# Optimization experiments

Measured on AMD Instinct MI355X. Metric: run time of the kernel, lower is better.

Reference implementation:

```python
import jax, jax.numpy as jnp
import numpy as np

B, S, E, H = 4, 2048, 2048, 16
D = E // H  # head_dim = 128


def setup_inputs() -> dict:
    key = jax.random.key(0)
    kx, kq, kk, kv = jax.random.split(key, 4)
    std = 1.0 / np.sqrt(E)
    return {
        "x": jax.random.normal(kx, (B, S, E), dtype=jnp.float32),
        "Wq": jax.random.normal(kq, (E, E), dtype=jnp.float32) * std,
        "Wk": jax.random.normal(kk, (E, E), dtype=jnp.float32) * std,
        "Wv": jax.random.normal(kv, (E, E), dtype=jnp.float32) * std,
    }


def reference(x, Wq, Wk, Wv):
    b, s, _ = x.shape
    # nn.Linear(bias=False): y = x @ W.T
    q = (x @ Wq.T).reshape(b, s, H, D).transpose(0, 2, 1, 3)  # [b,h,s,d]
    k = (x @ Wk.T).reshape(b, s, H, D).transpose(0, 2, 1, 3)
    v = (x @ Wv.T).reshape(b, s, H, D).transpose(0, 2, 1, 3)
    scale = jnp.sqrt(jnp.asarray(D, dtype=jnp.float32))
    scores = jnp.einsum("bhqd,bhkd->bhqk", q, k) / scale  # [b,h,s,s]
    causal = jnp.tril(jnp.ones((s, s), dtype=bool))
    scores = jnp.where(causal, scores, -jnp.inf)
    weights = jax.nn.softmax(scores, axis=-1)
    attn = jnp.einsum("bhqk,bhkd->bhqd", weights, v)  # [b,h,s,d]
    return attn
```

## Files before the change

### kernel.cpp

```cpp
#include <hip/hip_runtime.h>
#include <hip/hip_bf16.h>
#include <stdint.h>

#define Bdim 4
#define Sdim 2048
#define Edim 2048
#define Hdim 16
#define Ddim 128

typedef unsigned short u16;
typedef unsigned int u32;
typedef __attribute__((ext_vector_type(8))) short bf16x8;
typedef __attribute__((ext_vector_type(4))) float f32x4;
typedef __attribute__((ext_vector_type(16))) float f32x16;
typedef __attribute__((ext_vector_type(4))) unsigned short u16x4;
typedef __attribute__((ext_vector_type(2))) unsigned int u32x2;

__device__ inline u16 f2bf(float f) {
  union { float f; uint32_t u; } v; v.f = f;
  uint32_t u = v.u;
  return (u16)((u + 0x7FFFu + ((u >> 16) & 1u)) >> 16);
}

__device__ inline u32 pkbf(float lo, float hi) {
  float2 t; t.x = lo; t.y = hi;
  union { __hip_bfloat162 h2; u32 u; } cv;
  cv.h2 = __float22bfloat162_rn(t);
  return cv.u;
}

__device__ inline f32x4 mfma16(bf16x8 a, bf16x8 b, f32x4 c) {
  return __builtin_amdgcn_mfma_f32_16x16x32_bf16(a, b, c, 0, 0, 0);
}
__device__ inline f32x16 mfma32(bf16x8 a, bf16x8 b, f32x16 c) {
  return __builtin_amdgcn_mfma_f32_32x32x16_bf16(a, b, c, 0, 0, 0);
}

__device__ inline void load_lds16(const void* g, const void* l) {
  __builtin_amdgcn_global_load_lds(
      (__attribute__((address_space(1))) void*)(uintptr_t)g,
      (__attribute__((address_space(3))) void*)(uint32_t)(uintptr_t)l,
      16, 0, 0);
}

__global__ void cvt_kernel(const float* __restrict__ src, u16* __restrict__ dst,
                           int n4, float scale) {
  int i = blockIdx.x * blockDim.x + threadIdx.x;
  if (i < n4) {
    float4 f = ((const float4*)src)[i];
    u16x4 o = { f2bf(f.x * scale), f2bf(f.y * scale),
                f2bf(f.z * scale), f2bf(f.w * scale) };
    ((u16x4*)dst)[i] = o;
  }
}

__global__ void cvt_w_kernel(const float* __restrict__ Wq,
                             const float* __restrict__ Wk,
                             const float* __restrict__ Wv,
                             u16* __restrict__ dst, float qscale) {
  int i = blockIdx.x * blockDim.x + threadIdx.x;
  int seg = i >> 20;
  int off = i & 1048575;
  const float* src = seg == 0 ? Wq : (seg == 1 ? Wk : Wv);
  float sc = seg == 0 ? qscale : 1.0f;
  float4 f = ((const float4*)src)[off];
  u16x4 o = { f2bf(f.x * sc), f2bf(f.y * sc), f2bf(f.z * sc), f2bf(f.w * sc) };
  ((u16x4*)dst)[i] = o;
}

template <bool TRANSV>
__global__ __launch_bounds__(512, 2)
void gemm_nt(const u16* __restrict__ A, const u16* __restrict__ Bw,
             u16* __restrict__ C, int M, int N, int K) {
  __shared__ char lds[131072];

  const int tid = threadIdx.x;
  const int lane = tid & 63;
  const int w = tid >> 6;
  const int wm = w >> 2, wn = w & 3;
  const int bm = blockIdx.x, bn = blockIdx.y;
  const int NT = K >> 5;

  const int srow_off = lane >> 2;
  const int schunk = lane & 3;

  const int l15 = lane & 15;
  const int l4 = lane >> 4;
  const int rA = wm * 128 + l15;
  const int rB = wn * 64 + l15;
  const int gA = (rA + (rA >> 2)) & 3;
  const int gB = (rB + (rB >> 2)) & 3;
  const int aoff = rA * 64 + ((l4 ^ gA) << 4);
  const int boff = rB * 64 + ((l4 ^ gB) << 4);

  const u16* Agp = A + (size_t)(bm * 256) * K;
  const u16* Bgp = Bw + (size_t)(bn * 256) * K;

  f32x4 acc[8][4];
#pragma unroll
  for (int m = 0; m < 8; ++m)
#pragma unroll
    for (int n = 0; n < 4; ++n)
      acc[m][n] = (f32x4){0.f, 0.f, 0.f, 0.f};

#define GSTAGE_A(tt)                                                           \
  {                                                                            \
    char* ab_ = lds + ((tt) & 3) * 16384;                                      \
    _Pragma("unroll")                                                          \
    for (int i_ = 0; i_ < 2; ++i_) {                                           \
      const int rbase_ = w * 32 + i_ * 16;                                     \
      const int row_ = rbase_ + srow_off;                                      \
      const int src_ = schunk ^ ((row_ + (row_ >> 2)) & 3);                    \
      load_lds16(Agp + (size_t)row_ * K + (tt) * 32 + src_ * 8,                \
                 ab_ + rbase_ * 64);                                           \
    }                                                                          \
  }
#define GSTAGE_B(tt)                                                           \
  {                                                                            \
    char* bb_ = lds + 65536 + ((tt) & 3) * 16384;                              \
    _Pragma("unroll")                                                          \
    for (int i_ = 0; i_ < 2; ++i_) {                                           \
      const int rbase_ = w * 32 + i_ * 16;                                     \
      const int row_ = rbase_ + srow_off;                                      \
      const int src_ = schunk ^ ((row_ + (row_ >> 2)) & 3);                    \
      load_lds16(Bgp + (size_t)row_ * K + (tt) * 32 + src_ * 8,                \
                 bb_ + rbase_ * 64);                                           \
    }                                                                          \
  }

  GSTAGE_A(0); GSTAGE_B(0);
  GSTAGE_A(1); GSTAGE_B(1);
  asm volatile("s_waitcnt vmcnt(4)" ::: "memory");
  __builtin_amdgcn_s_barrier();

  for (int t = 0; t < NT; ++t) {
    const char* ab = lds + (t & 3) * 16384 + aoff;
    const char* bb = lds + 65536 + (t & 3) * 16384 + boff;
    const bool pf = (t + 2 < NT);

    bf16x8 bfr[4], afr[4];
#pragma unroll
    for (int n = 0; n < 4; ++n) bfr[n] = *(const bf16x8*)(bb + n * 1024);
#pragma unroll
    for (int m = 0; m < 4; ++m) afr[m] = *(const bf16x8*)(ab + m * 1024);
    if (pf) GSTAGE_A(t + 2);
    __builtin_amdgcn_s_barrier();
    __builtin_amdgcn_s_setprio(1);
#pragma unroll
    for (int m = 0; m < 4; ++m)
#pragma unroll
      for (int n = 0; n < 4; ++n) acc[m][n] = mfma16(afr[m], bfr[n], acc[m][n]);
    __builtin_amdgcn_s_setprio(0);
    __builtin_amdgcn_s_barrier();

#pragma unroll
    for (int m = 0; m < 4; ++m) afr[m] = *(const bf16x8*)(ab + (m + 4) * 1024);
    if (pf) GSTAGE_B(t + 2);
    __builtin_amdgcn_s_barrier();
    __builtin_amdgcn_s_setprio(1);
#pragma unroll
    for (int m = 0; m < 4; ++m)
#pragma unroll
      for (int n = 0; n < 4; ++n)
        acc[m + 4][n] = mfma16(afr[m], bfr[n], acc[m + 4][n]);
    __builtin_amdgcn_s_setprio(0);
    if (pf) {
      asm volatile("s_waitcnt vmcnt(4)" ::: "memory");
    } else {
      asm volatile("s_waitcnt vmcnt(0)" ::: "memory");
    }
    __builtin_amdgcn_s_barrier();
  }
#undef GSTAGE_A
#undef GSTAGE_B

  const int r0 = bm * 256 + wm * 128 + (l4 << 2);
  const int c0 = bn * 256 + wn * 64 + l15;
  if (!TRANSV) {
#pragma unroll
    for (int m = 0; m < 8; ++m)
#pragma unroll
      for (int n = 0; n < 4; ++n) {
        int r = r0 + m * 16;
        int c = c0 + n * 16;
#pragma unroll
        for (int j = 0; j < 4; ++j)
          C[(size_t)(r + j) * N + c] = f2bf(acc[m][n][j]);
      }
  } else {
#pragma unroll
    for (int m = 0; m < 8; ++m)
#pragma unroll
      for (int n = 0; n < 4; ++n) {
        int ng = c0 + n * 16;
        int h = ng >> 7, d = ng & 127;
        int mg = r0 + m * 16;
        int b = mg >> 11, s = mg & 2047;
        u16x4 pk = { f2bf(acc[m][n][0]), f2bf(acc[m][n][1]),
                     f2bf(acc[m][n][2]), f2bf(acc[m][n][3]) };
        *(u16x4*)(C + ((size_t)((b * Hdim + h) * Ddim + d)) * Sdim + s) = pk;
      }
  }
}

__global__ __launch_bounds__(256)
void attn_kernel(const u16* __restrict__ Q, const u16* __restrict__ K,
                 const u16* __restrict__ Vt, float* __restrict__ O) {
  __shared__ u16 Ks[2][64 * 128];
  __shared__ u16 Vs[2][128 * 64];

  const int tid = threadIdx.x;
  const int lane = tid & 63;
  const int w = tid >> 6;
  const int l31 = lane & 31;
  const int hi = lane >> 5;

  const int bid = blockIdx.x;
  const int bh = bid & 63;
  const int qg = 15 - (bid >> 6);
  const int q0 = qg * 128;
  const int qw0 = q0 + w * 32;
  const int b = bh >> 4, h = bh & 15;

  const u16* Qb = Q + (size_t)b * Sdim * Edim + h * Ddim;
  const u16* Kb = K + (size_t)b * Sdim * Edim + h * Ddim;
  const u16* Vb = Vt + (size_t)bh * Ddim * Sdim;

  bf16x8 qf[8];
  {
    const u16* qrow = Qb + (size_t)(qw0 + l31) * Edim + hi * 8;
#pragma unroll
    for (int c = 0; c < 8; ++c) qf[c] = *(const bf16x8*)(qrow + c * 16);
  }

  f32x16 oacc[4];
#pragma unroll
  for (int d = 0; d < 4; ++d)
#pragma unroll
    for (int i = 0; i < 16; ++i) oacc[d][i] = 0.f;
  f32x16 lacc;
#pragma unroll
  for (int i = 0; i < 16; ++i) lacc[i] = 0.f;

  const short oneb = (short)0x3F80;
  const bf16x8 ones = {oneb, oneb, oneb, oneb, oneb, oneb, oneb, oneb};

  float m2 = -1e30f;
  const int qrel = qw0 + l31;

  const int nt = 2 * qg + 2;
  const int ntw = (qw0 + 31) / 64 + 1;

  const int krow_off = (lane >> 4);
  const int kchunk = lane & 15;
  const int vrow_off = (lane >> 3);
  const int vchunk = lane & 7;

#define STAGE(bufi, tt)                                                        \
  {                                                                            \
    const int kv0s = (tt) * 64;                                                \
    _Pragma("unroll")                                                          \
    for (int i = 0; i < 4; ++i) {                                              \
      const int rbase = w * 16 + i * 4;                                        \
      const int row = rbase + krow_off;                                        \
      const int cs = kchunk ^ (row & 15);                                      \
      load_lds16(Kb + (size_t)(kv0s + row) * Edim + cs * 8,                    \
                 &Ks[bufi][rbase * 128]);                                      \
    }                                                                          \
    _Pragma("unroll")                                                          \
    for (int i = 0; i < 4; ++i) {                                              \
      const int rbase = w * 32 + i * 8;                                        \
      const int row = rbase + vrow_off;                                        \
      const int cs = vchunk ^ (row & 7);                                       \
      load_lds16(Vb + (size_t)row * Sdim + kv0s + cs * 8,                      \
                 &Vs[bufi][rbase * 64]);                                       \
    }                                                                          \
  }

  STAGE(0, 0);
  __syncthreads();

  for (int t = 0; t < nt; ++t) {
    const int cur = t & 1;
    if (t + 1 < nt) STAGE(cur ^ 1, t + 1);

    if (t < ntw) {
      const int kv0 = t * 64;

      f32x16 sc0, sc1;
#pragma unroll
      for (int i = 0; i < 16; ++i) { sc0[i] = 0.f; sc1[i] = 0.f; }
      __builtin_amdgcn_s_setprio(1);
#pragma unroll
      for (int c = 0; c < 8; ++c) {
        const int ch = c * 2 + hi;
        const int r0r = l31;
        const int r1r = 32 + l31;
        bf16x8 kf0 = *(const bf16x8*)&Ks[cur][r0r * 128 + (ch ^ (r0r & 15)) * 8];
        bf16x8 kf1 = *(const bf16x8*)&Ks[cur][r1r * 128 + (ch ^ (r1r & 15)) * 8];
        sc0 = mfma32(kf0, qf[c], sc0);
        sc1 = mfma32(kf1, qf[c], sc1);
      }
      __builtin_amdgcn_s_setprio(0);

      float psc[32];
      float ma = -1e30f, mb = -1e30f, mc = -1e30f, md = -1e30f;
      if (kv0 + 64 > qw0) {
#pragma unroll
        for (int r = 0; r < 16; ++r) {
          const int cr = (r & 3) + 8 * (r >> 2) + 4 * hi;
          float v0 = (kv0 + cr <= qrel) ? sc0[r] : -1e30f;
          float v1 = (kv0 + 32 + cr <= qrel) ? sc1[r] : -1e30f;
          psc[r] = v0; psc[16 + r] = v1;
          if ((r & 3) == 0) { ma = fmaxf(fmaxf(ma, v0), v1); }
          else if ((r & 3) == 1) { mb = fmaxf(fmaxf(mb, v0), v1); }
          else if ((r & 3) == 2) { mc = fmaxf(fmaxf(mc, v0), v1); }
          else { md = fmaxf(fmaxf(md, v0), v1); }
        }
      } else {
#pragma unroll
        for (int r = 0; r < 16; ++r) {
          float v0 = sc0[r];
          float v1 = sc1[r];
          psc[r] = v0; psc[16 + r] = v1;
          if ((r & 3) == 0) { ma = fmaxf(fmaxf(ma, v0), v1); }
          else if ((r & 3) == 1) { mb = fmaxf(fmaxf(mb, v0), v1); }
          else if ((r & 3) == 2) { mc = fmaxf(fmaxf(mc, v0), v1); }
          else { md = fmaxf(fmaxf(md, v0), v1); }
        }
      }
      float mt = fmaxf(fmaxf(ma, mb), fmaxf(mc, md));
      u32x2 mx = __builtin_amdgcn_permlane32_swap(
          __float_as_uint(mt), __float_as_uint(mt), false, false);
      float mo = fmaxf(__uint_as_float(mx.x), __uint_as_float(mx.y));

      if (__any(mo - m2 > 8.0f)) {
        float mnew = fmaxf(m2, mo);
        float corr = __builtin_amdgcn_exp2f(m2 - mnew);
        m2 = mnew;
        lacc[0] *= corr;
#pragma unroll
        for (int d = 0; d < 4; ++d)
#pragma unroll
          for (int i = 0; i < 16; ++i) oacc[d][i] *= corr;
      }

#pragma unroll
      for (int r = 0; r < 32; ++r)
        psc[r] = __builtin_amdgcn_exp2f(psc[r] - m2);

      u32 pk[16];
#pragma unroll
      for (int i = 0; i < 16; ++i) pk[i] = pkbf(psc[2 * i], psc[2 * i + 1]);
      bf16x8 pa[4];
#pragma unroll
      for (int t2 = 0; t2 < 2; ++t2)
#pragma unroll
        for (int q2 = 0; q2 < 2; ++q2) {
          const int base = t2 * 8 + q2 * 4;
          u32x2 r0 = __builtin_amdgcn_permlane32_swap(pk[base + 0], pk[base + 2],
                                                      false, false);
          u32x2 r1 = __builtin_amdgcn_permlane32_swap(pk[base + 1], pk[base + 3],
                                                      false, false);
          union { u32 wv[4]; bf16x8 v; } cv;
          cv.wv[0] = r0.x; cv.wv[1] = r1.x; cv.wv[2] = r0.y; cv.wv[3] = r1.y;
          pa[t2 * 2 + q2] = cv.v;
        }

      __builtin_amdgcn_s_setprio(1);
#pragma unroll
      for (int dblk = 0; dblk < 4; ++dblk) {
        const int row = dblk * 32 + l31;
#pragma unroll
        for (int ks = 0; ks < 4; ++ks) {
          const int ch = ks * 2 + hi;
          bf16x8 vf = *(const bf16x8*)&Vs[cur][row * 64 + (ch ^ (row & 7)) * 8];
          oacc[dblk] = mfma32(vf, pa[ks], oacc[dblk]);
        }
      }
#pragma unroll
      for (int ks = 0; ks < 4; ++ks) lacc = mfma32(ones, pa[ks], lacc);
      __builtin_amdgcn_s_setprio(0);
    }

    __syncthreads();
  }
#undef STAGE

  float inv = 1.0f / lacc[0];
  float* Ob = O + ((size_t)bh * Sdim + qw0 + l31) * Ddim + hi * 4;
#pragma unroll
  for (int dblk = 0; dblk < 4; ++dblk)
#pragma unroll
    for (int g = 0; g < 4; ++g) {
      f32x4 o4 = { oacc[dblk][4 * g] * inv, oacc[dblk][4 * g + 1] * inv,
                   oacc[dblk][4 * g + 2] * inv, oacc[dblk][4 * g + 3] * inv };
      *(f32x4*)(Ob + dblk * 32 + g * 8) = o4;
    }
}

extern "C" void kernel_launch(void* const* d_in, const int* in_sizes, int n_in,
                              void* d_out, int out_size, void* d_ws, size_t ws_size,
                              hipStream_t stream) {
  const float* x  = (const float*)d_in[0];
  const float* Wq = (const float*)d_in[1];
  const float* Wk = (const float*)d_in[2];
  const float* Wv = (const float*)d_in[3];
  float* out = (float*)d_out;
  char* ws = (char*)d_ws;

  u16* xb  = (u16*)(ws);
  u16* wqb = (u16*)(ws + 33554432ull);
  u16* wkb = (u16*)(ws + 41943040ull);
  u16* wvb = (u16*)(ws + 50331648ull);
  u16* Qb  = (u16*)(ws + 58720256ull);
  u16* Kb  = (u16*)(ws + 92274688ull);
  u16* Vt  = (u16*)(ws + 125829120ull);

  const int nX = Bdim * Sdim * Edim;
  const int nW = Edim * Edim;
  const float K1SC = 0.08838834764831845f * 1.4426950408889634f;
  cvt_kernel<<<(nX / 4 + 255) / 256, 256, 0, stream>>>(x, xb, nX / 4, 1.0f);
  cvt_w_kernel<<<(3 * nW / 4 + 255) / 256, 256, 0, stream>>>(Wq, Wk, Wv, wqb, K1SC);

  dim3 g(Bdim * Sdim / 256, Edim / 256);
  gemm_nt<false><<<g, 512, 0, stream>>>(xb, wqb, Qb, Bdim * Sdim, Edim, Edim);
  gemm_nt<false><<<g, 512, 0, stream>>>(xb, wkb, Kb, Bdim * Sdim, Edim, Edim);
  gemm_nt<true ><<<g, 512, 0, stream>>>(xb, wvb, Vt, Bdim * Sdim, Edim, Edim);

  attn_kernel<<<Bdim * Hdim * (Sdim / 128), 256, 0, stream>>>(Qb, Kb, Vt, out);
}
```

Baseline: 388.4 us.

## Restructure QKV GEMM to K=64 double-buffered quadrant pipeline, drop attention setprio

The projection GEMM now stages 64-wide K slices into two 64 KB buffers, each split into A and B halves. The loop is broken into four quadrant MFMA phases, each overlapped with a prefetch of one half-tile for the next step, and staggered vmcnt waits. This uses a new XOR swizzle over 8 chunks and an interleaved warp-to-row mapping, with a matching epilogue index change. The goal is fewer barriers per K element and better overlap of global-to-LDS loads with MFMA work. The s_setprio hints are also removed from the attention kernel, which could change how its waves are scheduled.

```diff
diff --git a/kernel.cpp b/kernel.cpp
--- a/kernel.cpp
+++ b/kernel.cpp
@@ -79,19 +79,19 @@
   const int w = tid >> 6;
   const int wm = w >> 2, wn = w & 3;
   const int bm = blockIdx.x, bn = blockIdx.y;
-  const int NT = K >> 5;
-
-  const int srow_off = lane >> 2;
-  const int schunk = lane & 3;
+  const int NT = K >> 6;
 
   const int l15 = lane & 15;
   const int l4 = lane >> 4;
-  const int rA = wm * 128 + l15;
-  const int rB = wn * 64 + l15;
-  const int gA = (rA + (rA >> 2)) & 3;
-  const int gB = (rB + (rB >> 2)) & 3;
-  const int aoff = rA * 64 + ((l4 ^ gA) << 4);
-  const int boff = rB * 64 + ((l4 ^ gB) << 4);
+  const int h7 = l15 & 7;
+
+  const int srow = lane >> 3;
+  const int schunk = (lane & 7) ^ srow;
+
+  const int ck0 = (l4 ^ h7) << 4;
+  const int ck1 = ((4 + l4) ^ h7) << 4;
+  const int arow0 = (wm * 16 + l15) * 128;
+  const int brow0 = (wn * 16 + l15) * 128;
 
   const u16* Agp = A + (size_t)(bm * 256) * K;
   const u16* Bgp = Bw + (size_t)(bn * 256) * K;
@@ -103,104 +103,129 @@
     for (int n = 0; n < 4; ++n)
       acc[m][n] = (f32x4){0.f, 0.f, 0.f, 0.f};
 
-#define GSTAGE_A(tt)                                                           \
+#define STG_A(hh, tt)                                                          \
   {                                                                            \
-    char* ab_ = lds + ((tt) & 3) * 16384;                                      \
+    char* d_ = lds + ((tt) & 1) * 65536 + (hh) * 16384;                        \
     _Pragma("unroll")                                                          \
-    for (int i_ = 0; i_ < 2; ++i_) {                                           \
-      const int rbase_ = w * 32 + i_ * 16;                                     \
-      const int row_ = rbase_ + srow_off;                                      \
-      const int src_ = schunk ^ ((row_ + (row_ >> 2)) & 3);                    \
-      load_lds16(Agp + (size_t)row_ * K + (tt) * 32 + src_ * 8,                \
-                 ab_ + rbase_ * 64);                                           \
-    }                                                                          \
-  }
-#define GSTAGE_B(tt)                                                           \
+    for (int i_ = 0; i_ < 2; ++i_)                                             \
+      load_lds16(Agp + (size_t)((hh) * 128 + w * 8 + srow + i_ * 64) * K +     \
+                     (tt) * 64 + schunk * 8,                                   \
+                 d_ + (w * 8 + i_ * 64) * 128);                                \
+  }
+#define STG_B(hh, tt)                                                          \
   {                                                                            \
-    char* bb_ = lds + 65536 + ((tt) & 3) * 16384;                              \
+    char* d_ = lds + ((tt) & 1) * 65536 + 32768 + (hh) * 16384;                \
     _Pragma("unroll")                                                          \
-    for (int i_ = 0; i_ < 2; ++i_) {                                           \
-      const int rbase_ = w * 32 + i_ * 16;                                     \
-      const int row_ = rbase_ + srow_off;                                      \
-      const int src_ = schunk ^ ((row_ + (row_ >> 2)) & 3);                    \
-      load_lds16(Bgp + (size_t)row_ * K + (tt) * 32 + src_ * 8,                \
-                 bb_ + rbase_ * 64);                                           \
-    }                                                                          \
-  }
-
-  GSTAGE_A(0); GSTAGE_B(0);
-  GSTAGE_A(1); GSTAGE_B(1);
-  asm volatile("s_waitcnt vmcnt(4)" ::: "memory");
+    for (int i_ = 0; i_ < 2; ++i_)                                             \
+      load_lds16(Bgp + (size_t)((hh) * 128 + w * 8 + srow + i_ * 64) * K +     \
+                     (tt) * 64 + schunk * 8,                                   \
+                 d_ + (w * 8 + i_ * 64) * 128);                                \
+  }
+
+  STG_A(0, 0); STG_B(0, 0); STG_B(1, 0); STG_A(1, 0);
+  asm volatile("s_waitcnt vmcnt(0)" ::: "memory");
   __builtin_amdgcn_s_barrier();
 
   for (int t = 0; t < NT; ++t) {
-    const char* ab = lds + (t & 3) * 16384 + aoff;
-    const char* bb = lds + 65536 + (t & 3) * 16384 + boff;
-    const bool pf = (t + 2 < NT);
-
-    bf16x8 bfr[4], afr[4];
-#pragma unroll
-    for (int n = 0; n < 4; ++n) bfr[n] = *(const bf16x8*)(bb + n * 1024);
-#pragma unroll
-    for (int m = 0; m < 4; ++m) afr[m] = *(const bf16x8*)(ab + m * 1024);
-    if (pf) GSTAGE_A(t + 2);
+    const char* bc = lds + (t & 1) * 65536;
+    const bool pf = (t + 1 < NT);
+
+    if (pf) STG_A(0, t + 1);
+    bf16x8 a0[4][2], b0[2][2];
+#pragma unroll
+    for (int q = 0; q < 4; ++q) {
+      a0[q][0] = *(const bf16x8*)(bc + arow0 + q * 4096 + ck0);
+      a0[q][1] = *(const bf16x8*)(bc + arow0 + q * 4096 + ck1);
+    }
+#pragma unroll
+    for (int n = 0; n < 2; ++n) {
+      b0[n][0] = *(const bf16x8*)(bc + 32768 + brow0 + n * 8192 + ck0);
+      b0[n][1] = *(const bf16x8*)(bc + 32768 + brow0 + n * 8192 + ck1);
+    }
+    __builtin_amdgcn_s_setprio(1);
+#pragma unroll
+    for (int q = 0; q < 4; ++q)
+#pragma unroll
+      for (int n = 0; n < 2; ++n) {
+        acc[q][n] = mfma16(a0[q][0], b0[n][0], acc[q][n]);
+        acc[q][n] = mfma16(a0[q][1], b0[n][1], acc[q][n]);
+      }
+    __builtin_amdgcn_s_setprio(0);
+    asm volatile("s_waitcnt vmcnt(4)" ::: "memory");
     __builtin_amdgcn_s_barrier();
+
+    if (pf) STG_B(0, t + 1);
+    bf16x8 b1[2][2];
+#pragma unroll
+    for (int n = 0; n < 2; ++n) {
+      b1[n][0] = *(const bf16x8*)(bc + 49152 + brow0 + n * 8192 + ck0);
+      b1[n][1] = *(const bf16x8*)(bc + 49152 + brow0 + n * 8192 + ck1);
+    }
     __builtin_amdgcn_s_setprio(1);
 #pragma unroll
-    for (int m = 0; m < 4; ++m)
-#pragma unroll
-      for (int n = 0; n < 4; ++n) acc[m][n] = mfma16(afr[m], bfr[n], acc[m][n]);
+    for (int q = 0; q < 4; ++q)
+#pragma unroll
+      for (int n = 0; n < 2; ++n) {
+        acc[q][n + 2] = mfma16(a0[q][0], b1[n][0], acc[q][n + 2]);
+        acc[q][n + 2] = mfma16(a0[q][1], b1[n][1], acc[q][n + 2]);
+      }
     __builtin_amdgcn_s_setprio(0);
+    asm volatile("s_waitcnt vmcnt(4)" ::: "memory");
     __builtin_amdgcn_s_barrier();
 
-#pragma unroll
-    for (int m = 0; m < 4; ++m) afr[m] = *(const bf16x8*)(ab + (m + 4) * 1024);
-    if (pf) GSTAGE_B(t + 2);
+    if (pf) STG_B(1, t + 1);
+    bf16x8 a1[4][2];
+#pragma unroll
+    for (int q = 0; q < 4; ++q) {
+      a1[q][0] = *(const bf16x8*)(bc + 16384 + arow0 + q * 4096 + ck0);
+      a1[q][1] = *(const bf16x8*)(bc + 16384 + arow0 + q * 4096 + ck1);
+    }
+    __builtin_amdgcn_s_setprio(1);
+#pragma unroll
+    for (int q = 0; q < 4; ++q)
+#pragma unroll
+      for (int n = 0; n < 2; ++n) {
+        acc[q + 4][n + 2] = mfma16(a1[q][0], b1[n][0], acc[q + 4][n + 2]);
+        acc[q + 4][n + 2] = mfma16(a1[q][1], b1[n][1], acc[q + 4][n + 2]);
+      }
+    __builtin_amdgcn_s_setprio(0);
+    asm volatile("s_waitcnt vmcnt(6)" ::: "memory");
     __builtin_amdgcn_s_barrier();
+
+    if (pf) STG_A(1, t + 1);
     __builtin_amdgcn_s_setprio(1);
 #pragma unroll
-    for (int m = 0; m < 4; ++m)
-#pragma unroll
-      for (int n = 0; n < 4; ++n)
-        acc[m + 4][n] = mfma16(afr[m], bfr[n], acc[m + 4][n]);
+    for (int q = 0; q < 4; ++q)
+#pragma unroll
+      for (int n = 0; n < 2; ++n) {
+        acc[q + 4][n] = mfma16(a1[q][0], b0[n][0], acc[q + 4][n]);
+        acc[q + 4][n] = mfma16(a1[q][1], b0[n][1], acc[q + 4][n]);
+      }
     __builtin_amdgcn_s_setprio(0);
-    if (pf) {
-      asm volatile("s_waitcnt vmcnt(4)" ::: "memory");
-    } else {
-      asm volatile("s_waitcnt vmcnt(0)" ::: "memory");
-    }
+    asm volatile("s_waitcnt vmcnt(4)" ::: "memory");
     __builtin_amdgcn_s_barrier();
   }
-#undef GSTAGE_A
-#undef GSTAGE_B
-
-  const int r0 = bm * 256 + wm * 128 + (l4 << 2);
-  const int c0 = bn * 256 + wn * 64 + l15;
-  if (!TRANSV) {
-#pragma unroll
-    for (int m = 0; m < 8; ++m)
-#pragma unroll
-      for (int n = 0; n < 4; ++n) {
-        int r = r0 + m * 16;
-        int c = c0 + n * 16;
+#undef STG_A
+#undef STG_B
+
+#pragma unroll
+  for (int m = 0; m < 8; ++m)
+#pragma unroll
+    for (int n = 0; n < 4; ++n) {
+      int r = bm * 256 + (m & 3) * 32 + wm * 16 + (m >> 2) * 128 + (l4 << 2);
+      int c = bn * 256 + (n & 1) * 64 + wn * 16 + (n >> 1) * 128 + l15;
+      if (!TRANSV) {
 #pragma unroll
         for (int j = 0; j < 4; ++j)
           C[(size_t)(r + j) * N + c] = f2bf(acc[m][n][j]);
-      }
-  } else {
-#pragma unroll
-    for (int m = 0; m < 8; ++m)
-#pragma unroll
-      for (int n = 0; n < 4; ++n) {
-        int ng = c0 + n * 16;
-        int h = ng >> 7, d = ng & 127;
-        int mg = r0 + m * 16;
-        int b = mg >> 11, s = mg & 2047;
+      } else {
+        int h = c >> 7, d = c & 127;
+        int b = r >> 11, s = r & 2047;
         u16x4 pk = { f2bf(acc[m][n][0]), f2bf(acc[m][n][1]),
                      f2bf(acc[m][n][2]), f2bf(acc[m][n][3]) };
         *(u16x4*)(C + ((size_t)((b * Hdim + h) * Ddim + d)) * Sdim + s) = pk;
       }
-  }
+    }
 }
 
 __global__ __launch_bounds__(256)
@@ -290,7 +315,6 @@
       f32x16 sc0, sc1;
 #pragma unroll
       for (int i = 0; i < 16; ++i) { sc0[i] = 0.f; sc1[i] = 0.f; }
-      __builtin_amdgcn_s_setprio(1);
 #pragma unroll
       for (int c = 0; c < 8; ++c) {
         const int ch = c * 2 + hi;
@@ -301,7 +325,6 @@
         sc0 = mfma32(kf0, qf[c], sc0);
         sc1 = mfma32(kf1, qf[c], sc1);
       }
-      __builtin_amdgcn_s_setprio(0);
 
       float psc[32];
       float ma = -1e30f, mb = -1e30f, mc = -1e30f, md = -1e30f;
@@ -367,7 +390,6 @@
           pa[t2 * 2 + q2] = cv.v;
         }
 
-      __builtin_amdgcn_s_setprio(1);
 #pragma unroll
       for (int dblk = 0; dblk < 4; ++dblk) {
         const int row = dblk * 32 + l31;
@@ -380,7 +402,6 @@
       }
 #pragma unroll
       for (int ks = 0; ks < 4; ++ks) lacc = mfma32(ones, pa[ks], lacc);
-      __builtin_amdgcn_s_setprio(0);
     }
 
     __syncthreads();
```

After: 362.7 us, median of 4. -6.6%, faster.
